# Kernel optimization log

Measured on AMD Instinct MI355X. Metric: run time of the kernel, lower is better.

The kernel has to match this reference:

```python
import jax, jax.numpy as jnp
import numpy as np

B, L, D, A, OUT, HID_FC = 4, 4096, 128, 16, 2, 24


def setup_inputs() -> dict:
    key = jax.random.key(0)
    ks = jax.random.split(key, 8)
    xn = lambda k, shape: (jax.random.normal(k, shape, dtype=jnp.float32)
                           * np.sqrt(2.0 / (shape[0] + shape[1])))
    return {
        "x": jax.random.normal(ks[0], (B, L, D), dtype=jnp.float32),
        "fc1_w": xn(ks[1], (D, D)),
        "fc1_b": jnp.zeros((D,), dtype=jnp.float32),
        "Wq_w": xn(ks[2], (D, D)),
        "Wk_w": xn(ks[3], (D, D)),
        "Wv_w": xn(ks[4], (D, D)),
        "fc2_w": xn(ks[5], (D, HID_FC)),
        "fc2_b": jnp.zeros((HID_FC,), dtype=jnp.float32),
        "fc3_w": xn(ks[6], (HID_FC, OUT)),
        "fc3_b": jnp.zeros((OUT,), dtype=jnp.float32),
        "atten_size": A,
        "hidden_size": D,
    }


def _attention(x, Wq_w, Wk_w, Wv_w, atten_size, sqrt_hidden):
    b, l, d = x.shape
    W = 2 * atten_size + 1
    # zero-pad sequence dim, then gather local windows.
    # Faithful to roll-based construction: x_nei[b,i,j] = x[b, i + atten_size - j] (0 if out of range)
    padded = jnp.pad(x, ((0, 0), (atten_size, atten_size), (0, 0)))
    idx = jnp.arange(l)[:, None] + 2 * atten_size - jnp.arange(W)[None, :]  # [L, W]
    x_nei = padded[:, idx]                      # [B, L, W, D]
    q = (x @ Wq_w)[:, :, None, :]               # [B, L, 1, D]
    k = x_nei @ Wk_w                            # [B, L, W, D]
    dsc = jnp.einsum('blod,blwd->blow', q, k) / sqrt_hidden  # [B, L, 1, W]
    # Original torch code: Softmax(dim=2) over the singleton dim -> all-ones (faithful)
    a = jax.nn.softmax(dsc, axis=2)             # [B, L, 1, W]
    v = x_nei @ Wv_w                            # [B, L, W, D]
    out = jnp.squeeze(a @ v, axis=2)            # [B, L, D]
    return out, a


def reference(x, fc1_w, fc1_b, Wq_w, Wk_w, Wv_w, fc2_w, fc2_b, fc3_w, fc3_b,
              atten_size, hidden_size):
    sqrt_hidden = np.sqrt(float(hidden_size))
    h = jax.nn.relu(x @ fc1_w + fc1_b)
    h, a = _attention(h, Wq_w, Wk_w, Wv_w, atten_size, sqrt_hidden)
    h = jax.nn.relu(h @ fc2_w + fc2_b)
    out = h @ fc3_w + fc3_b
    return out, a
```

## Files before the change

kernel.cpp:

```cpp
#include <hip/hip_runtime.h>

constexpr int Bv   = 4;
constexpr int Lv   = 4096;
constexpr int Dv   = 128;
constexpr int Av   = 16;
constexpr int Wwin = 2*Av + 1;
constexpr int OUTv = 2;
constexpr int HIDv = 24;
constexpr int NROWS = Bv * Lv;

constexpr int TILE  = 32;
constexpr int SROWS = TILE + 2*Av;
constexpr int NBLK  = NROWS / TILE;
constexpr int NT    = 512;

typedef __attribute__((ext_vector_type(8))) short short8;
typedef __attribute__((ext_vector_type(4))) short short4v;
typedef __attribute__((ext_vector_type(4))) float f32x4;

__device__ __forceinline__ short f2bf(float f) {
    unsigned u = __builtin_bit_cast(unsigned, f);
    u += 0x7FFFu + ((u >> 16) & 1u);
    return (short)(u >> 16);
}

__global__ __launch_bounds__(NT) void k_all(const float* __restrict__ x,
                                            const float* __restrict__ W1,
                                            const float* __restrict__ b1,
                                            const float* __restrict__ Wv,
                                            const float* __restrict__ fc2,
                                            const float* __restrict__ fc2b,
                                            const float* __restrict__ fc3w,
                                            const float* __restrict__ fc3b,
                                            float* __restrict__ out,
                                            float* __restrict__ aout) {
    __shared__ short sA[SROWS][136];
    __shared__ short sH[SROWS][136];
    __shared__ short sWfT[32][136];
    __shared__ float smv[SROWS][25];
    __shared__ float sh2[TILE][25];
    __shared__ float sb1[Dv];

    const int t = threadIdx.x, blk = blockIdx.x;
    const int g0 = blk * TILE;
    const int bb = g0 >> 12;
    const int l0 = g0 & (Lv - 1);
    const int lane = t & 63, w = t >> 6;
    const int arow = lane & 15;
    const int kgrp = (lane >> 4) * 8;
    const int crow = (lane >> 4) * 4;
    const int ncol0 = w * 16;

    for (int i = t; i < SROWS*32; i += NT) {
        const int r = i >> 5, c4 = i & 31;
        const int l = l0 - Av + r;
        short4v o = {0, 0, 0, 0};
        if (l >= 0 && l < Lv) {
            const float4 v = *(const float4*)&x[((size_t)bb*Lv + l)*Dv + c4*4];
            o[0] = f2bf(v.x); o[1] = f2bf(v.y); o[2] = f2bf(v.z); o[3] = f2bf(v.w);
        }
        *(short4v*)&sA[r][c4*4] = o;
    }
    if (t < Dv) sb1[t] = b1[t];

    if (t < 264) {
        const float4 one4 = {1.f, 1.f, 1.f, 1.f};
        ((float4*)aout)[(size_t)blk*264 + t] = one4;
    }

    short8 pb[4];
    {
        const int n0 = ncol0 + arow;
#pragma unroll
        for (int kb = 0; kb < 4; ++kb) {
            const int kof = kb*32 + kgrp;
            float a0[8];
#pragma unroll
            for (int j = 0; j < 8; ++j)
                a0[j] = W1[(size_t)(kof + j)*Dv + n0];
            short8 b0;
#pragma unroll
            for (int j = 0; j < 8; ++j) b0[j] = f2bf(a0[j]);
            pb[kb] = b0;
        }
    }

    {
        f32x4 accW[2];
        accW[0] = (f32x4){0,0,0,0};
        accW[1] = (f32x4){0,0,0,0};
#pragma unroll
        for (int kb = 0; kb < 4; ++kb) {
            const int kof = kb*32 + kgrp;
            const int m = w*16 + arow;
            const float4 v0 = *(const float4*)&Wv[(size_t)m*Dv + kof];
            const float4 v1 = *(const float4*)&Wv[(size_t)m*Dv + kof + 4];
            short8 aW;
            aW[0] = f2bf(v0.x); aW[1] = f2bf(v0.y); aW[2] = f2bf(v0.z); aW[3] = f2bf(v0.w);
            aW[4] = f2bf(v1.x); aW[5] = f2bf(v1.y); aW[6] = f2bf(v1.z); aW[7] = f2bf(v1.w);
#pragma unroll
            for (int nf = 0; nf < 2; ++nf) {
                const int n = nf*16 + arow;
                short8 bW;
#pragma unroll
                for (int j = 0; j < 8; ++j) {
                    const float v = (n < HIDv) ? fc2[(size_t)(kof + j)*HIDv + n] : 0.f;
                    bW[j] = f2bf(v);
                }
                accW[nf] = __builtin_amdgcn_mfma_f32_16x16x32_bf16(aW, bW, accW[nf], 0, 0, 0);
            }
        }
#pragma unroll
        for (int nf = 0; nf < 2; ++nf) {
            const int n = nf*16 + arow;
            const int m = w*16 + crow;
            short4v o;
            o[0] = f2bf(accW[nf][0]);
            o[1] = f2bf(accW[nf][1]);
            o[2] = f2bf(accW[nf][2]);
            o[3] = f2bf(accW[nf][3]);
            *(short4v*)&sWfT[n][m] = o;
        }
    }
    __syncthreads();

    {
        f32x4 acc[4];
#pragma unroll
        for (int mf = 0; mf < 4; ++mf) acc[mf] = (f32x4){0,0,0,0};

#pragma unroll
        for (int kb = 0; kb < 4; ++kb) {
            const int kof = kb*32 + kgrp;
#pragma unroll
            for (int mf = 0; mf < 4; ++mf) {
                const short8 af = *(const short8*)&sA[mf*16 + arow][kof];
                acc[mf] = __builtin_amdgcn_mfma_f32_16x16x32_bf16(af, pb[kb], acc[mf], 0, 0, 0);
            }
        }

        const int col  = ncol0 + arow;
        const float bias = sb1[col];
#pragma unroll
        for (int mf = 0; mf < 4; ++mf) {
#pragma unroll
            for (int r = 0; r < 4; ++r) {
                float h = acc[mf][r] + bias;
                h = h > 0.f ? h : 0.f;
                sH[mf*16 + crow + r][col] = f2bf(h);
            }
        }
    }
    __syncthreads();

    {
        const int mf = w >> 1, nf = w & 1;
        f32x4 acc2 = (f32x4){0,0,0,0};
#pragma unroll
        for (int kb = 0; kb < 4; ++kb) {
            const int kof = kb*32 + kgrp;
            const short8 af = *(const short8*)&sH[mf*16 + arow][kof];
            const short8 bf = *(const short8*)&sWfT[nf*16 + arow][kof];
            acc2 = __builtin_amdgcn_mfma_f32_16x16x32_bf16(af, bf, acc2, 0, 0, 0);
        }
        const int col = nf*16 + arow;
        if (col < HIDv) {
#pragma unroll
            for (int r = 0; r < 4; ++r) {
                const int row = mf*16 + crow + r;
                const int l = l0 - Av + row;
                smv[row][col] = (l >= 0 && l < Lv) ? acc2[r] : 0.f;
            }
        }
    }
    __syncthreads();

    for (int i = t; i < TILE*HIDv; i += NT) {
        const int r = i / HIDv, c = i % HIDv;
        float s = 0.f;
#pragma unroll
        for (int ww = 0; ww < Wwin; ++ww) s += smv[r + ww][c];
        const float h = s + fc2b[c];
        sh2[r][c] = h > 0.f ? h : 0.f;
    }
    __syncthreads();

    if (t < TILE*OUTv) {
        const int r = t >> 1, oc = t & 1;
        float a = fc3b[oc];
#pragma unroll
        for (int c = 0; c < HIDv; ++c)
            a = fmaf(sh2[r][c], fc3w[c*OUTv + oc], a);
        out[(size_t)(g0 + r)*OUTv + oc] = a;
    }
}

extern "C" void kernel_launch(void* const* d_in, const int* in_sizes, int n_in,
                              void* d_out, int out_size, void* d_ws, size_t ws_size,
                              hipStream_t stream) {
    const float* x     = (const float*)d_in[0];
    const float* fc1_w = (const float*)d_in[1];
    const float* fc1_b = (const float*)d_in[2];
    const float* Wv_w  = (const float*)d_in[5];
    const float* fc2_w = (const float*)d_in[6];
    const float* fc2_b = (const float*)d_in[7];
    const float* fc3_w = (const float*)d_in[8];
    const float* fc3_b = (const float*)d_in[9];

    float* out  = (float*)d_out;
    float* aout = (float*)d_out + NROWS * OUTv;

    k_all<<<dim3(NBLK), dim3(NT), 0, stream>>>(x, fc1_w, fc1_b, Wv_w, fc2_w,
                                               fc2_b, fc3_w, fc3_b, out, aout);
}
```

Before: 17.64 us.

## Double row tile to 64 to cut halo recompute and move fc1 weight loads into loop

Raises the per-block row tile from 32 to 64, so each block computes 96 rows (64 plus a 32-row halo) instead of 64, which lowers the share of redundant halo fc1/Wv work and halves the number of blocks. The fc1 weight fragment loads now happen inside the k-loop instead of being preloaded, and the all-ones attention output writes move to after the first GEMM. The second GEMM is spread across six waves with two tiles each. The trade-off is fewer blocks (256) on a large GPU, which may leave compute units underused, plus more LDS per block.

```diff
diff --git a/kernel.cpp b/kernel.cpp
--- a/kernel.cpp
+++ b/kernel.cpp
@@ -9,7 +9,7 @@
 constexpr int HIDv = 24;
 constexpr int NROWS = Bv * Lv;
 
-constexpr int TILE  = 32;
+constexpr int TILE  = 64;
 constexpr int SROWS = TILE + 2*Av;
 constexpr int NBLK  = NROWS / TILE;
 constexpr int NT    = 512;
@@ -63,28 +63,6 @@
     }
     if (t < Dv) sb1[t] = b1[t];
 
-    if (t < 264) {
-        const float4 one4 = {1.f, 1.f, 1.f, 1.f};
-        ((float4*)aout)[(size_t)blk*264 + t] = one4;
-    }
-
-    short8 pb[4];
-    {
-        const int n0 = ncol0 + arow;
-#pragma unroll
-        for (int kb = 0; kb < 4; ++kb) {
-            const int kof = kb*32 + kgrp;
-            float a0[8];
-#pragma unroll
-            for (int j = 0; j < 8; ++j)
-                a0[j] = W1[(size_t)(kof + j)*Dv + n0];
-            short8 b0;
-#pragma unroll
-            for (int j = 0; j < 8; ++j) b0[j] = f2bf(a0[j]);
-            pb[kb] = b0;
-        }
-    }
-
     {
         f32x4 accW[2];
         accW[0] = (f32x4){0,0,0,0};
@@ -125,24 +103,32 @@
     __syncthreads();
 
     {
-        f32x4 acc[4];
-#pragma unroll
-        for (int mf = 0; mf < 4; ++mf) acc[mf] = (f32x4){0,0,0,0};
-
+        f32x4 acc[6];
+#pragma unroll
+        for (int mf = 0; mf < 6; ++mf) acc[mf] = (f32x4){0,0,0,0};
+
+        const int n0 = ncol0 + arow;
 #pragma unroll
         for (int kb = 0; kb < 4; ++kb) {
             const int kof = kb*32 + kgrp;
-#pragma unroll
-            for (int mf = 0; mf < 4; ++mf) {
+            float a0[8];
+#pragma unroll
+            for (int j = 0; j < 8; ++j)
+                a0[j] = W1[(size_t)(kof + j)*Dv + n0];
+            short8 bf;
+#pragma unroll
+            for (int j = 0; j < 8; ++j) bf[j] = f2bf(a0[j]);
+#pragma unroll
+            for (int mf = 0; mf < 6; ++mf) {
                 const short8 af = *(const short8*)&sA[mf*16 + arow][kof];
-                acc[mf] = __builtin_amdgcn_mfma_f32_16x16x32_bf16(af, pb[kb], acc[mf], 0, 0, 0);
+                acc[mf] = __builtin_amdgcn_mfma_f32_16x16x32_bf16(af, bf, acc[mf], 0, 0, 0);
             }
         }
 
         const int col  = ncol0 + arow;
         const float bias = sb1[col];
 #pragma unroll
-        for (int mf = 0; mf < 4; ++mf) {
+        for (int mf = 0; mf < 6; ++mf) {
 #pragma unroll
             for (int r = 0; r < 4; ++r) {
                 float h = acc[mf][r] + bias;
@@ -153,23 +139,37 @@
     }
     __syncthreads();
 
-    {
-        const int mf = w >> 1, nf = w & 1;
-        f32x4 acc2 = (f32x4){0,0,0,0};
-#pragma unroll
-        for (int kb = 0; kb < 4; ++kb) {
-            const int kof = kb*32 + kgrp;
-            const short8 af = *(const short8*)&sH[mf*16 + arow][kof];
-            const short8 bf = *(const short8*)&sWfT[nf*16 + arow][kof];
-            acc2 = __builtin_amdgcn_mfma_f32_16x16x32_bf16(af, bf, acc2, 0, 0, 0);
-        }
-        const int col = nf*16 + arow;
-        if (col < HIDv) {
-#pragma unroll
-            for (int r = 0; r < 4; ++r) {
-                const int row = mf*16 + crow + r;
-                const int l = l0 - Av + row;
-                smv[row][col] = (l >= 0 && l < Lv) ? acc2[r] : 0.f;
+    for (int i = t; i < 528; i += NT) {
+        const float4 one4 = {1.f, 1.f, 1.f, 1.f};
+        ((float4*)aout)[(size_t)blk*528 + i] = one4;
+    }
+
+    if (w < 6) {
+        f32x4 acc2[2];
+        acc2[0] = (f32x4){0,0,0,0};
+        acc2[1] = (f32x4){0,0,0,0};
+#pragma unroll
+        for (int pp = 0; pp < 2; ++pp) {
+            const int p = w*2 + pp, mf = p >> 1, nf = p & 1;
+#pragma unroll
+            for (int kb = 0; kb < 4; ++kb) {
+                const int kof = kb*32 + kgrp;
+                const short8 af = *(const short8*)&sH[mf*16 + arow][kof];
+                const short8 bf = *(const short8*)&sWfT[nf*16 + arow][kof];
+                acc2[pp] = __builtin_amdgcn_mfma_f32_16x16x32_bf16(af, bf, acc2[pp], 0, 0, 0);
+            }
+        }
+#pragma unroll
+        for (int pp = 0; pp < 2; ++pp) {
+            const int p = w*2 + pp, mf = p >> 1, nf = p & 1;
+            const int col = nf*16 + arow;
+            if (col < HIDv) {
+#pragma unroll
+                for (int r = 0; r < 4; ++r) {
+                    const int row = mf*16 + crow + r;
+                    const int l = l0 - Av + row;
+                    smv[row][col] = (l >= 0 && l < Lv) ? acc2[pp][r] : 0.f;
+                }
             }
         }
     }
```

New measurement: 14.79 us, median of 2. 1.19x faster.
